# Performance work log

Measured on AMD Instinct MI355X. Metric: run time of the kernel, lower is better.

Reference implementation:

```python
import math
import jax, jax.numpy as jnp
import numpy as np

EMB_DIM = 1024
CFG_N_HEADS = 16
# Faithful to the torch module: n_heads collapses to 1 when config.n_heads < emb_dim
N_HEADS = CFG_N_HEADS if CFG_N_HEADS >= EMB_DIM else 1


def setup_inputs() -> dict:
    key = jax.random.key(0)
    ks = jax.random.split(key, 11)
    B, T, C = 4, 2048, EMB_DIM
    s = 1.0 / math.sqrt(C)
    return {
        "q": jax.random.normal(ks[0], (B, T, C), jnp.float32),
        "k": jax.random.normal(ks[1], (B, T, C), jnp.float32),
        "v": jax.random.normal(ks[2], (B, T, C), jnp.float32),
        "Wq": jax.random.normal(ks[3], (C, C), jnp.float32) * s,
        "bq": jax.random.normal(ks[4], (C,), jnp.float32) * s,
        "Wk": jax.random.normal(ks[5], (C, C), jnp.float32) * s,
        "bk": jax.random.normal(ks[6], (C,), jnp.float32) * s,
        "Wv": jax.random.normal(ks[7], (C, C), jnp.float32) * s,
        "bv": jax.random.normal(ks[8], (C,), jnp.float32) * s,
        "Wff": jax.random.normal(ks[9], (C, C), jnp.float32) * s,
        "bff": jax.random.normal(ks[10], (C,), jnp.float32) * s,
    }


def reference(q, k, v, Wq, bq, Wk, bk, Wv, bv, Wff, bff):
    B, T, C = q.shape
    H = N_HEADS
    D = C // H  # head dim (== C here since H degenerates to 1)
    # torch Linear: x @ W.T + b
    qp = (q @ Wq.T + bq).reshape(B, T, H, D).transpose(0, 2, 1, 3)  # [B,H,T,D]
    kp = (k @ Wk.T + bk).reshape(B, T, H, D).transpose(0, 2, 1, 3)
    vp = (v @ Wv.T + bv).reshape(B, T, H, D).transpose(0, 2, 1, 3)
    scale = 1.0 / math.sqrt(D)
    scores = jnp.einsum('bhqd,bhkd->bhqk', qp, kp) * scale  # [B,H,T,T]
    causal = jnp.tril(jnp.ones((T, T), dtype=bool))
    scores = jnp.where(causal[None, None, :, :], scores, -jnp.inf)
    attn = jax.nn.softmax(scores, axis=-1)
    out = jnp.einsum('bhqk,bhkd->bhqd', attn, vp)  # [B,H,T,D]
    out = out.transpose(0, 2, 1, 3).reshape(B, T, C)
    return out @ Wff.T + bff
```

## Files before the change

kernel.cpp:

```cpp
#include <hip/hip_runtime.h>
#include <stdint.h>

typedef unsigned short u16;
typedef short v8s __attribute__((ext_vector_type(8)));
typedef float v4f __attribute__((ext_vector_type(4)));

#define BM 128
#define BN 128
#define BK 64

__device__ __forceinline__ float b2f(u16 b) {
  union { unsigned u; float f; } x; x.u = ((unsigned)b) << 16; return x.f;
}
__device__ __forceinline__ u16 f2b(float f) {
  union { float f; unsigned u; } x; x.f = f;
  unsigned r = x.u + 0x7fffu + ((x.u >> 16) & 1u);
  return (u16)(r >> 16);
}

__device__ __forceinline__ void async_copy16(const void* g, void* lds) {
  __builtin_amdgcn_global_load_lds(
      (const __attribute__((address_space(1))) void*)g,
      (__attribute__((address_space(3))) void*)(uint32_t)(uintptr_t)lds,
      16, 0, 0);
}

__device__ __forceinline__ void xcd_swz(int& bx, int& by) {
  const int gx = gridDim.x;
  const int nwg = gx * gridDim.y;
  const int ord = blockIdx.y * gx + blockIdx.x;
  const int q = nwg >> 3, r = nwg & 7;
  const int xcd = ord & 7, local = ord >> 3;
  const int base = xcd < r ? xcd * (q + 1) : r * (q + 1) + (xcd - r) * q;
  const int s = base + local;
  bx = s % gx;
  by = s / gx;
}

__device__ __forceinline__ void causal_pair_swz(int& bx, int& by) {
  const int gx = gridDim.x;
  const int ord = blockIdx.y * gx + blockIdx.x;
  const int k = ord & 7;
  const int j = ord >> 3;
  by = (j < gx) ? k : 15 - k;
  bx = (j < gx) ? j : j - gx;
}

__global__ __launch_bounds__(256) void cvt_all_kernel(
    const float* __restrict__ i0, const float* __restrict__ i1,
    const float* __restrict__ i2, const float* __restrict__ i3,
    const float* __restrict__ i4, const float* __restrict__ i5,
    const float* __restrict__ i6, u16* __restrict__ o0, u16* __restrict__ o1,
    u16* __restrict__ o2, u16* __restrict__ o3, u16* __restrict__ o4,
    u16* __restrict__ o5, u16* __restrict__ o6, int n_big, int n_small) {
  const int z = blockIdx.y;
  const float* in;
  u16* out;
  int n;
  switch (z) {
    case 0: in = i0; out = o0; n = n_big; break;
    case 1: in = i1; out = o1; n = n_big; break;
    case 2: in = i2; out = o2; n = n_big; break;
    case 3: in = i3; out = o3; n = n_small; break;
    case 4: in = i4; out = o4; n = n_small; break;
    case 5: in = i5; out = o5; n = n_small; break;
    default: in = i6; out = o6; n = n_small; break;
  }
  const int i = (blockIdx.x * 256 + threadIdx.x) * 8;
  if (i >= n) return;
  v4f a = *(const v4f*)(in + i);
  v4f b = *(const v4f*)(in + i + 4);
  v8s o;
#pragma unroll
  for (int j = 0; j < 4; j++) o[j] = (short)f2b(a[j]);
#pragma unroll
  for (int j = 0; j < 4; j++) o[4 + j] = (short)f2b(b[j]);
  *(v8s*)(out + i) = o;
}

union LdsU {
  struct { u16 a[BM * BK]; u16 b[BN * BK]; } s;
  u16 t[128 * 136];
};

template <bool HAS_BIAS, bool CAUSAL_K, bool OUT_F32, bool TR_OUT>
__device__ __forceinline__ void gemm_body(
    LdsU& lds, const u16* __restrict__ A, int lda,
    const u16* __restrict__ Bm, int ldb, void* __restrict__ Cout_, int ldc,
    long cbase, const float* __restrict__ bias, int K, int m0, int n0) {
  u16* ldsA = lds.s.a;
  u16* ldsB = lds.s.b;

  const int tid = threadIdx.x;
  const int wave = tid >> 6, lane = tid & 63;
  const int wm = (wave >> 1) * 64, wn = (wave & 1) * 64;
  const int lrow = lane & 15, quad = lane >> 4;

  v4f acc[4][4];
#pragma unroll
  for (int i = 0; i < 4; i++)
#pragma unroll
    for (int j = 0; j < 4; j++) acc[i][j] = v4f{0.f, 0.f, 0.f, 0.f};

  int Keff = K;
  if (CAUSAL_K) {
    int ke = m0 + BM;
    Keff = ke < K ? ke : K;
  }

  const int rA = lane >> 3;
  const int uch = (lane & 7) ^ rA;
  const u16* pA = A + (long)(m0 + wave * 8 + rA) * lda + uch * 8;
  const u16* pB = Bm + (long)(n0 + wave * 8 + rA) * ldb + uch * 8;
  u16* dA = ldsA + (wave * 8) * BK;
  u16* dB = ldsB + (wave * 8) * BK;

  for (int k0 = 0; k0 < Keff; k0 += BK) {
#pragma unroll
    for (int c = 0; c < 4; c++) {
      async_copy16(pA + (long)c * 32 * lda + k0, dA + c * 32 * BK);
      async_copy16(pB + (long)c * 32 * ldb + k0, dB + c * 32 * BK);
    }
    __syncthreads();

#pragma unroll
    for (int ks = 0; ks < 2; ks++) {
      v8s af[4], bfr[4];
#pragma unroll
      for (int mt = 0; mt < 4; mt++) {
        const int r = wm + mt * 16 + lrow;
        af[mt] =
            *(const v8s*)&ldsA[r * BK + ((ks * 4 + quad) ^ (r & 7)) * 8];
      }
#pragma unroll
      for (int nt = 0; nt < 4; nt++) {
        const int r = wn + nt * 16 + lrow;
        bfr[nt] =
            *(const v8s*)&ldsB[r * BK + ((ks * 4 + quad) ^ (r & 7)) * 8];
      }
#pragma unroll
      for (int mt = 0; mt < 4; mt++)
#pragma unroll
        for (int nt = 0; nt < 4; nt++)
          acc[mt][nt] = __builtin_amdgcn_mfma_f32_16x16x32_bf16(
              af[mt], bfr[nt], acc[mt][nt], 0, 0, 0);
    }
    __syncthreads();
  }

  if (TR_OUT) {
#pragma unroll
    for (int mt = 0; mt < 4; mt++) {
      const int rl = wm + mt * 16 + quad * 4;
#pragma unroll
      for (int nt = 0; nt < 4; nt++) {
        const int cl = wn + nt * 16 + lrow;
        float bv = 0.f;
        if (HAS_BIAS) bv = bias[n0 + cl];
#pragma unroll
        for (int i = 0; i < 4; i++)
          lds.t[cl * 136 + rl + i] = f2b(acc[mt][nt][i] + bv);
      }
    }
    __syncthreads();
    const int cl2 = tid >> 1, th = (tid & 1) * 64;
    const long bbase =
        (long)(m0 >> 11) * ((long)1024 * 2048) + (long)(m0 & 2047);
    u16* dst = (u16*)Cout_ + bbase + (long)(n0 + cl2) * 2048 + th;
    const u16* srcl = &lds.t[cl2 * 136 + th];
#pragma unroll
    for (int j = 0; j < 8; j++)
      *(v8s*)(dst + j * 8) = *(const v8s*)(srcl + j * 8);
    return;
  }

#pragma unroll
  for (int mt = 0; mt < 4; mt++) {
    const int rowBase = m0 + wm + mt * 16 + quad * 4;
#pragma unroll
    for (int nt = 0; nt < 4; nt++) {
      const int col = n0 + wn + nt * 16 + lrow;
      float bv = 0.f;
      if (HAS_BIAS) bv = bias[col];
#pragma unroll
      for (int i = 0; i < 4; i++) {
        const long idx = cbase + (long)(rowBase + i) * ldc + col;
        const float val = acc[mt][nt][i] + bv;
        if (OUT_F32)
          ((float*)Cout_)[idx] = val;
        else
          ((u16*)Cout_)[idx] = f2b(val);
      }
    }
  }
}

__global__ __launch_bounds__(256, 4) void qkv_gemm_kernel(
    const u16* __restrict__ a0, const u16* __restrict__ a1,
    const u16* __restrict__ a2, const u16* __restrict__ w0,
    const u16* __restrict__ w1, const u16* __restrict__ w2,
    const float* __restrict__ b0, const float* __restrict__ b1,
    const float* __restrict__ b2, u16* __restrict__ c0, u16* __restrict__ c1,
    u16* __restrict__ c2, int C) {
  __shared__ LdsU lds;
  const int z = blockIdx.z;
  const u16* A = z == 0 ? a0 : (z == 1 ? a1 : a2);
  const u16* W = z == 0 ? w0 : (z == 1 ? w1 : w2);
  const float* bias = z == 0 ? b0 : (z == 1 ? b1 : b2);
  u16* Cp = z == 0 ? c0 : (z == 1 ? c1 : c2);
  int bx, by;
  xcd_swz(bx, by);
  if (z == 2)
    gemm_body<true, false, false, true>(lds, A, C, W, C, Cp, C, 0, bias, C,
                                        by * BM, bx * BN);
  else
    gemm_body<true, false, false, false>(lds, A, C, W, C, Cp, C, 0, bias, C,
                                         by * BM, bx * BN);
}

template <bool HAS_BIAS, bool CAUSAL_SKIP, bool CAUSAL_K, bool OUT_F32,
          int SWZ>
__global__ __launch_bounds__(256, 4) void gemm_bt_kernel(
    const u16* __restrict__ A, int lda, long sA,
    const u16* __restrict__ Bm, int ldb, long sB,
    void* __restrict__ Cout_, int ldc, long sC,
    const float* __restrict__ bias, int K) {
  __shared__ LdsU lds;
  int bx, by;
  if (SWZ == 1)
    causal_pair_swz(bx, by);
  else
    xcd_swz(bx, by);
  const int m0 = by * BM;
  const int n0 = bx * BN;
  if (CAUSAL_SKIP && n0 > m0) return;
  const int z = blockIdx.z;
  gemm_body<HAS_BIAS, CAUSAL_K, OUT_F32, false>(
      lds, A + (long)z * sA, lda, Bm + (long)z * sB, ldb, Cout_, ldc,
      (long)z * sC, bias, K, m0, n0);
}

__global__ __launch_bounds__(256) void softmax_kernel(u16* __restrict__ S) {
  const float scale = 0.03125f;
  const int wave = threadIdx.x >> 6, lane = threadIdx.x & 63;
  const int i = blockIdx.x * 4 + wave, b = blockIdx.y;
  u16* row = S + ((long)b * 2048 + (long)i) * 2048;
  const int Lw = ((i >> 7) + 1) << 7;
  float v[32];
  float m = -1e30f;
#pragma unroll
  for (int c = 0; c < 4; c++) {
    const int jb = c * 512 + lane * 8;
    v8s raw = {0, 0, 0, 0, 0, 0, 0, 0};
    if (jb <= i) raw = *(const v8s*)&row[jb];
#pragma unroll
    for (int jj = 0; jj < 8; jj++) {
      float x = (jb + jj <= i) ? b2f((u16)raw[jj]) * scale : -1e30f;
      v[c * 8 + jj] = x;
      m = fmaxf(m, x);
    }
  }
#pragma unroll
  for (int off = 32; off; off >>= 1) m = fmaxf(m, __shfl_xor(m, off));
  float s = 0.f;
#pragma unroll
  for (int c = 0; c < 4; c++)
#pragma unroll
    for (int jj = 0; jj < 8; jj++) {
      float e = (v[c * 8 + jj] > -1e29f) ? __expf(v[c * 8 + jj] - m) : 0.f;
      v[c * 8 + jj] = e;
      s += e;
    }
#pragma unroll
  for (int off = 32; off; off >>= 1) s += __shfl_xor(s, off);
  const float inv = 1.0f / s;
#pragma unroll
  for (int c = 0; c < 4; c++) {
    const int jb = c * 512 + lane * 8;
    if (jb < Lw) {
      v8s o;
#pragma unroll
      for (int jj = 0; jj < 8; jj++) o[jj] = (short)f2b(v[c * 8 + jj] * inv);
      *(v8s*)&row[jb] = o;
    }
  }
}

extern "C" void kernel_launch(void* const* d_in, const int* in_sizes, int n_in,
                              void* d_out, int out_size, void* d_ws,
                              size_t ws_size, hipStream_t stream) {
  const float* q = (const float*)d_in[0];
  const float* k = (const float*)d_in[1];
  const float* v = (const float*)d_in[2];
  const float* Wq = (const float*)d_in[3];
  const float* bq = (const float*)d_in[4];
  const float* Wk = (const float*)d_in[5];
  const float* bk = (const float*)d_in[6];
  const float* Wv = (const float*)d_in[7];
  const float* bv = (const float*)d_in[8];
  const float* Wff = (const float*)d_in[9];
  const float* bff = (const float*)d_in[10];
  float* out = (float*)d_out;

  const int B = 4, T = 2048, C = 1024, M = B * T;
  const size_t MC = (size_t)M * C;
  const size_t CC = (size_t)C * C;
  u16* ws = (u16*)d_ws;
  u16* qb = ws;
  u16* kb = qb + MC;
  u16* vb = kb + MC;
  u16* Wqb = vb + MC;
  u16* Wkb = Wqb + CC;
  u16* Wvb = Wkb + CC;
  u16* Wffb = Wvb + CC;
  u16* Qp = Wffb + CC;
  u16* Kp = Qp + MC;
  u16* Vp = Kp + MC;
  u16* VpT = Vp + MC;
  u16* S = qb;
  u16* attn = Vp;

  dim3 blk(256);
  cvt_all_kernel<<<dim3((int)(MC / 2048), 7), blk, 0, stream>>>(
      q, k, v, Wq, Wk, Wv, Wff, qb, kb, vb, Wqb, Wkb, Wvb, Wffb,
      (int)MC, (int)CC);

  qkv_gemm_kernel<<<dim3(C / BN, M / BM, 3), blk, 0, stream>>>(
      qb, kb, vb, Wqb, Wkb, Wvb, bq, bk, bv, Qp, Kp, VpT, C);
  gemm_bt_kernel<false, true, false, false, 1>
      <<<dim3(T / BN, T / BM, B), blk, 0, stream>>>(
          Qp, C, (long)T * C, Kp, C, (long)T * C, S, T, (long)T * T,
          nullptr, C);
  softmax_kernel<<<dim3(T / 4, B), blk, 0, stream>>>(S);
  gemm_bt_kernel<false, false, true, false, 1>
      <<<dim3(C / BN, T / BM, B), blk, 0, stream>>>(
          S, T, (long)T * T, VpT, T, (long)C * T, attn, C, (long)T * C,
          nullptr, T);
  gemm_bt_kernel<true, false, false, true, 0>
      <<<dim3(C / BN, M / BM, 1), blk, 0, stream>>>(
          attn, C, 0, Wffb, C, 0, out, C, 0, bff, C);
}
```

Baseline: 326.3 us.

## Fuse causal softmax into QK^T epilogue and normalize in PV epilogue

Removes the separate softmax kernel. The QK^T GEMM epilogue now writes unnormalized exp(score*scale) with the causal mask applied, and accumulates per-row sums into a float buffer through shuffles and atomicAdd. The PV GEMM epilogue divides by that row sum. The row-sum buffer is zeroed inside the existing conversion kernel, and the generic GEMM kernel drops the transpose LDS union to use less shared memory. This saves a full read/write pass over the score matrix, but exponentiates without subtracting the row max, so it can overflow for large-magnitude scores; it also adds atomics.

```diff
diff --git a/kernel.cpp b/kernel.cpp
--- a/kernel.cpp
+++ b/kernel.cpp
@@ -3,6 +3,7 @@
 
 typedef unsigned short u16;
 typedef short v8s __attribute__((ext_vector_type(8)));
+typedef short s4 __attribute__((ext_vector_type(4)));
 typedef float v4f __attribute__((ext_vector_type(4)));
 
 #define BM 128
@@ -52,8 +53,14 @@
     const float* __restrict__ i4, const float* __restrict__ i5,
     const float* __restrict__ i6, u16* __restrict__ o0, u16* __restrict__ o1,
     u16* __restrict__ o2, u16* __restrict__ o3, u16* __restrict__ o4,
-    u16* __restrict__ o5, u16* __restrict__ o6, int n_big, int n_small) {
+    u16* __restrict__ o5, u16* __restrict__ o6, u16* __restrict__ o7,
+    int n_big, int n_small, int n_l) {
   const int z = blockIdx.y;
+  const int i = (blockIdx.x * 256 + threadIdx.x) * 8;
+  if (z == 7) {
+    if (i < n_l) *(v8s*)(o7 + i) = v8s{0, 0, 0, 0, 0, 0, 0, 0};
+    return;
+  }
   const float* in;
   u16* out;
   int n;
@@ -66,7 +73,6 @@
     case 5: in = i5; out = o5; n = n_small; break;
     default: in = i6; out = o6; n = n_small; break;
   }
-  const int i = (blockIdx.x * 256 + threadIdx.x) * 8;
   if (i >= n) return;
   v4f a = *(const v4f*)(in + i);
   v4f b = *(const v4f*)(in + i + 4);
@@ -78,19 +84,19 @@
   *(v8s*)(out + i) = o;
 }
 
+struct LdsS { u16 a[BM * BK]; u16 b[BN * BK]; };
 union LdsU {
-  struct { u16 a[BM * BK]; u16 b[BN * BK]; } s;
+  LdsS s;
   u16 t[128 * 136];
 };
 
-template <bool HAS_BIAS, bool CAUSAL_K, bool OUT_F32, bool TR_OUT>
+template <bool HAS_BIAS, bool CAUSAL_K, bool OUT_F32, bool TR_OUT,
+          bool EXP_OUT, bool NORM_L>
 __device__ __forceinline__ void gemm_body(
-    LdsU& lds, const u16* __restrict__ A, int lda,
+    u16* ldsA, u16* ldsB, u16* ldsT, const u16* __restrict__ A, int lda,
     const u16* __restrict__ Bm, int ldb, void* __restrict__ Cout_, int ldc,
-    long cbase, const float* __restrict__ bias, int K, int m0, int n0) {
-  u16* ldsA = lds.s.a;
-  u16* ldsB = lds.s.b;
-
+    long cbase, const float* __restrict__ bias, float* __restrict__ lsum,
+    int K, int m0, int n0) {
   const int tid = threadIdx.x;
   const int wave = tid >> 6, lane = tid & 63;
   const int wm = (wave >> 1) * 64, wn = (wave & 1) * 64;
@@ -157,9 +163,10 @@
         const int cl = wn + nt * 16 + lrow;
         float bv = 0.f;
         if (HAS_BIAS) bv = bias[n0 + cl];
-#pragma unroll
-        for (int i = 0; i < 4; i++)
-          lds.t[cl * 136 + rl + i] = f2b(acc[mt][nt][i] + bv);
+        s4 w;
+#pragma unroll
+        for (int i = 0; i < 4; i++) w[i] = (short)f2b(acc[mt][nt][i] + bv);
+        *(s4*)&ldsT[cl * 136 + rl] = w;
       }
     }
     __syncthreads();
@@ -167,10 +174,55 @@
     const long bbase =
         (long)(m0 >> 11) * ((long)1024 * 2048) + (long)(m0 & 2047);
     u16* dst = (u16*)Cout_ + bbase + (long)(n0 + cl2) * 2048 + th;
-    const u16* srcl = &lds.t[cl2 * 136 + th];
+    const u16* srcl = &ldsT[cl2 * 136 + th];
 #pragma unroll
     for (int j = 0; j < 8; j++)
       *(v8s*)(dst + j * 8) = *(const v8s*)(srcl + j * 8);
+    return;
+  }
+
+  if (EXP_OUT) {
+    const float scale = 0.03125f;
+#pragma unroll
+    for (int mt = 0; mt < 4; mt++) {
+      const int rowBase = m0 + wm + mt * 16 + quad * 4;
+#pragma unroll
+      for (int i = 0; i < 4; i++) {
+        const int row = rowBase + i;
+        float part = 0.f;
+#pragma unroll
+        for (int nt = 0; nt < 4; nt++) {
+          const int col = n0 + wn + nt * 16 + lrow;
+          float e = 0.f;
+          if (col <= row) e = __expf(acc[mt][nt][i] * scale);
+          part += e;
+          ((u16*)Cout_)[cbase + (long)row * ldc + col] = f2b(e);
+        }
+        part += __shfl_xor(part, 1);
+        part += __shfl_xor(part, 2);
+        part += __shfl_xor(part, 4);
+        part += __shfl_xor(part, 8);
+        if (lrow == 0) atomicAdd(&lsum[row], part);
+      }
+    }
+    return;
+  }
+
+  if (NORM_L) {
+#pragma unroll
+    for (int mt = 0; mt < 4; mt++) {
+      const int rowBase = m0 + wm + mt * 16 + quad * 4;
+#pragma unroll
+      for (int i = 0; i < 4; i++) {
+        const float inv = 1.0f / lsum[rowBase + i];
+#pragma unroll
+        for (int nt = 0; nt < 4; nt++) {
+          const int col = n0 + wn + nt * 16 + lrow;
+          ((u16*)Cout_)[cbase + (long)(rowBase + i) * ldc + col] =
+              f2b(acc[mt][nt][i] * inv);
+        }
+      }
+    }
     return;
   }
 
@@ -211,21 +263,23 @@
   int bx, by;
   xcd_swz(bx, by);
   if (z == 2)
-    gemm_body<true, false, false, true>(lds, A, C, W, C, Cp, C, 0, bias, C,
-                                        by * BM, bx * BN);
+    gemm_body<true, false, false, true, false, false>(
+        lds.s.a, lds.s.b, lds.t, A, C, W, C, Cp, C, 0, bias, nullptr, C,
+        by * BM, bx * BN);
   else
-    gemm_body<true, false, false, false>(lds, A, C, W, C, Cp, C, 0, bias, C,
-                                         by * BM, bx * BN);
+    gemm_body<true, false, false, false, false, false>(
+        lds.s.a, lds.s.b, nullptr, A, C, W, C, Cp, C, 0, bias, nullptr, C,
+        by * BM, bx * BN);
 }
 
 template <bool HAS_BIAS, bool CAUSAL_SKIP, bool CAUSAL_K, bool OUT_F32,
-          int SWZ>
+          int SWZ, bool EXP_OUT, bool NORM_L>
 __global__ __launch_bounds__(256, 4) void gemm_bt_kernel(
     const u16* __restrict__ A, int lda, long sA,
     const u16* __restrict__ Bm, int ldb, long sB,
     void* __restrict__ Cout_, int ldc, long sC,
-    const float* __restrict__ bias, int K) {
-  __shared__ LdsU lds;
+    const float* __restrict__ bias, float* __restrict__ lsum, int K) {
+  __shared__ LdsS lds;
   int bx, by;
   if (SWZ == 1)
     causal_pair_swz(bx, by);
@@ -235,55 +289,10 @@
   const int n0 = bx * BN;
   if (CAUSAL_SKIP && n0 > m0) return;
   const int z = blockIdx.z;
-  gemm_body<HAS_BIAS, CAUSAL_K, OUT_F32, false>(
-      lds, A + (long)z * sA, lda, Bm + (long)z * sB, ldb, Cout_, ldc,
-      (long)z * sC, bias, K, m0, n0);
-}
-
-__global__ __launch_bounds__(256) void softmax_kernel(u16* __restrict__ S) {
-  const float scale = 0.03125f;
-  const int wave = threadIdx.x >> 6, lane = threadIdx.x & 63;
-  const int i = blockIdx.x * 4 + wave, b = blockIdx.y;
-  u16* row = S + ((long)b * 2048 + (long)i) * 2048;
-  const int Lw = ((i >> 7) + 1) << 7;
-  float v[32];
-  float m = -1e30f;
-#pragma unroll
-  for (int c = 0; c < 4; c++) {
-    const int jb = c * 512 + lane * 8;
-    v8s raw = {0, 0, 0, 0, 0, 0, 0, 0};
-    if (jb <= i) raw = *(const v8s*)&row[jb];
-#pragma unroll
-    for (int jj = 0; jj < 8; jj++) {
-      float x = (jb + jj <= i) ? b2f((u16)raw[jj]) * scale : -1e30f;
-      v[c * 8 + jj] = x;
-      m = fmaxf(m, x);
-    }
-  }
-#pragma unroll
-  for (int off = 32; off; off >>= 1) m = fmaxf(m, __shfl_xor(m, off));
-  float s = 0.f;
-#pragma unroll
-  for (int c = 0; c < 4; c++)
-#pragma unroll
-    for (int jj = 0; jj < 8; jj++) {
-      float e = (v[c * 8 + jj] > -1e29f) ? __expf(v[c * 8 + jj] - m) : 0.f;
-      v[c * 8 + jj] = e;
-      s += e;
-    }
-#pragma unroll
-  for (int off = 32; off; off >>= 1) s += __shfl_xor(s, off);
-  const float inv = 1.0f / s;
-#pragma unroll
-  for (int c = 0; c < 4; c++) {
-    const int jb = c * 512 + lane * 8;
-    if (jb < Lw) {
-      v8s o;
-#pragma unroll
-      for (int jj = 0; jj < 8; jj++) o[jj] = (short)f2b(v[c * 8 + jj] * inv);
-      *(v8s*)&row[jb] = o;
-    }
-  }
+  gemm_body<HAS_BIAS, CAUSAL_K, OUT_F32, false, EXP_OUT, NORM_L>(
+      lds.a, lds.b, nullptr, A + (long)z * sA, lda, Bm + (long)z * sB, ldb,
+      Cout_, ldc, (long)z * sC, bias,
+      lsum ? lsum + (long)z * 2048 : nullptr, K, m0, n0);
 }
 
 extern "C" void kernel_launch(void* const* d_in, const int* in_sizes, int n_in,
@@ -317,26 +326,26 @@
   u16* Kp = Qp + MC;
   u16* Vp = Kp + MC;
   u16* VpT = Vp + MC;
+  float* lsum = (float*)(VpT + MC);
   u16* S = qb;
   u16* attn = Vp;
 
   dim3 blk(256);
-  cvt_all_kernel<<<dim3((int)(MC / 2048), 7), blk, 0, stream>>>(
+  cvt_all_kernel<<<dim3((int)(MC / 2048), 8), blk, 0, stream>>>(
       q, k, v, Wq, Wk, Wv, Wff, qb, kb, vb, Wqb, Wkb, Wvb, Wffb,
-      (int)MC, (int)CC);
+      (u16*)lsum, (int)MC, (int)CC, B * T * 2);
 
   qkv_gemm_kernel<<<dim3(C / BN, M / BM, 3), blk, 0, stream>>>(
       qb, kb, vb, Wqb, Wkb, Wvb, bq, bk, bv, Qp, Kp, VpT, C);
-  gemm_bt_kernel<false, true, false, false, 1>
+  gemm_bt_kernel<false, true, false, false, 1, true, false>
       <<<dim3(T / BN, T / BM, B), blk, 0, stream>>>(
           Qp, C, (long)T * C, Kp, C, (long)T * C, S, T, (long)T * T,
-          nullptr, C);
-  softmax_kernel<<<dim3(T / 4, B), blk, 0, stream>>>(S);
-  gemm_bt_kernel<false, false, true, false, 1>
+          nullptr, lsum, C);
+  gemm_bt_kernel<false, false, true, false, 1, false, true>
       <<<dim3(C / BN, T / BM, B), blk, 0, stream>>>(
           S, T, (long)T * T, VpT, T, (long)C * T, attn, C, (long)T * C,
-          nullptr, T);
-  gemm_bt_kernel<true, false, false, true, 0>
+          nullptr, lsum, T);
+  gemm_bt_kernel<true, false, false, true, 0, false, false>
       <<<dim3(C / BN, M / BM, 1), blk, 0, stream>>>(
-          attn, C, 0, Wffb, C, 0, out, C, 0, bff, C);
-}
+          attn, C, 0, Wffb, C, 0, out, C, 0, bff, nullptr, C);
+}
```

Result: faster. 318.3 us (-2.4%).
